# Kernel tuning notes

Hardware: AMD Instinct MI355X
Metric: run time of the kernel (lower is better)

The kernel has to match this reference:

```python
import jax, jax.numpy as jnp
import numpy as np

N = 50000       # nodes
E = 500000      # edges
F_IN = 64       # input feature dim
F_OUT = 64      # hidden/output dim
K = 3           # diffusion filter order
C = F_IN + F_OUT  # concat dim seen by each DConv


def _xavier(k, shape):
    fan_in, fan_out = shape[-2], shape[-1]
    lim = float(np.sqrt(6.0 / (fan_in + fan_out)))
    return jax.random.uniform(k, shape, jnp.float32, -lim, lim)


def setup_inputs() -> dict:
    key = jax.random.key(0)
    ks = jax.random.split(key, 8)
    X = jax.random.normal(ks[0], (N, F_IN), jnp.float32)
    H = jax.random.normal(ks[1], (N, F_OUT), jnp.float32)
    # ring edges guarantee every node has in-degree >= 1 and out-degree >= 1
    base = jnp.arange(N, dtype=jnp.int32)
    row = jnp.concatenate([base, jax.random.randint(ks[2], (E - N,), 0, N, jnp.int32)])
    col = jnp.concatenate([jnp.roll(base, 1), jax.random.randint(ks[3], (E - N,), 0, N, jnp.int32)])
    edge_index = jnp.stack([row, col])  # [2, E]
    W_z = _xavier(ks[4], (2, K, C, F_OUT))
    W_r = _xavier(ks[5], (2, K, C, F_OUT))
    W_h = _xavier(ks[6], (2, K, C, F_OUT))
    b = jnp.zeros((F_OUT,), jnp.float32)
    return {"X": X, "edge_index": edge_index, "H": H,
            "W_z": W_z, "b_z": b, "W_r": W_r, "b_r": b, "W_h": W_h, "b_h": b}


def _dconv(Xc, row, col, norm_out, norm_in, W, b):
    # PyG propagate: gather source (row) features, scale by edge norm, scatter-add to target (col)
    def prop(x, norm):
        return jax.ops.segment_sum(norm[:, None] * x[row], col, num_segments=N)
    Tx_0 = Xc
    Hout = Xc @ (W[0, 0] + W[1, 0])
    Tx_1_o = prop(Xc, norm_out)
    Tx_1_i = prop(Xc, norm_in)
    Hout = Hout + Tx_1_o @ W[0, 1] + Tx_1_i @ W[1, 1]
    for k in range(2, K):
        Tx_2_o = 2.0 * prop(Tx_1_o, norm_out) - Tx_0
        Tx_2_i = 2.0 * prop(Tx_1_i, norm_in) - Tx_0
        Hout = Hout + Tx_2_o @ W[0, k] + Tx_2_i @ W[1, k]
        # faithful to original: Tx_1 is never reassigned, so Tx_0 stays Xc
        Tx_0, Tx_1_o, Tx_1_i = Xc, Tx_2_o, Tx_2_i
    return Hout + b


def reference(X, edge_index, H, W_z, b_z, W_r, b_r, W_h, b_h):
    row, col = edge_index[0], edge_index[1]
    deg_out = jnp.zeros((N,), jnp.float32).at[row].add(1.0)
    deg_in = jnp.zeros((N,), jnp.float32).at[col].add(1.0)
    norm_out = (1.0 / deg_out)[row]
    norm_in = (1.0 / deg_in)[row]
    XH = jnp.concatenate([X, H], axis=1)
    Z = jax.nn.sigmoid(_dconv(XH, row, col, norm_out, norm_in, W_z, b_z))
    R = jax.nn.sigmoid(_dconv(XH, row, col, norm_out, norm_in, W_r, b_r))
    XHR = jnp.concatenate([X, H * R], axis=1)
    H_tilde = jnp.tanh(_dconv(XHR, row, col, norm_out, norm_in, W_h, b_h))
    H_new = Z * H + (1.0 - Z) * H_tilde
    # NaN infill with mean of non-NaN entries (faithful to original)
    mask = jnp.isnan(H_new)
    H_new = jnp.where(mask, jnp.nanmean(H_new), H_new)
    return H_new
```

## Files before the change

kernel.cpp:

```cpp
#include <hip/hip_runtime.h>
#include <hip/hip_bf16.h>
#include <math.h>

#define N_NODES 50000
#define N_EDGES 500000
#define C_DIM 128
#define N_TILES 3125

#define CSR_BLOCKS 1954
#define CONCAT_BLOCKS 3125
#define PACK_BLOCKS 480

typedef __attribute__((ext_vector_type(8))) short bf8;
typedef __attribute__((ext_vector_type(4))) float f32x4;
typedef __attribute__((ext_vector_type(2))) float f32x2;

__device__ __forceinline__ float bflo(unsigned u) { return __uint_as_float(u << 16); }
__device__ __forceinline__ float bfhi(unsigned u) { return __uint_as_float(u & 0xffff0000u); }
__device__ __forceinline__ unsigned short f2bfu(float f) {
    __hip_bfloat16 h = __float2bfloat16(f);
    unsigned short u;
    __builtin_memcpy(&u, &h, 2);
    return u;
}
__device__ __forceinline__ unsigned packbf(float a, float b) {
    return ((unsigned)f2bfu(b) << 16) | f2bfu(a);
}


__global__ void count_deg(const int* __restrict__ row, const int* __restrict__ col,
                          int* __restrict__ dout, int* __restrict__ din, int e) {
    int i = blockIdx.x * blockDim.x + threadIdx.x;
    if (i >= e) return;
    atomicAdd(&dout[row[i]], 1);
    atomicAdd(&din[col[i]], 1);
}

__global__ void scan_block(const int* __restrict__ counts, int* __restrict__ excl,
                           int* __restrict__ blocksums, int n) {
    __shared__ int tmp[1024];
    int tid = threadIdx.x;
    int gid = blockIdx.x * 1024 + tid;
    int v = (gid < n) ? counts[gid] : 0;
    tmp[tid] = v;
    __syncthreads();
    for (int off = 1; off < 1024; off <<= 1) {
        int t = (tid >= off) ? tmp[tid - off] : 0;
        __syncthreads();
        tmp[tid] += t;
        __syncthreads();
    }
    int incl = tmp[tid];
    if (gid < n) excl[gid] = incl - v;
    if (tid == 1023) blocksums[blockIdx.x] = incl;
}

__global__ void scan_sums(int* __restrict__ blocksums, int nb) {
    __shared__ int tmp[64];
    int tid = threadIdx.x;
    int v = (tid < nb) ? blocksums[tid] : 0;
    tmp[tid] = v;
    __syncthreads();
    for (int off = 1; off < 64; off <<= 1) {
        int t = (tid >= off) ? tmp[tid - off] : 0;
        __syncthreads();
        tmp[tid] += t;
        __syncthreads();
    }
    if (tid < nb) blocksums[tid] = tmp[tid] - v;
}

__global__ void scan_add(int* __restrict__ rowptr, const int* __restrict__ blocksums,
                         int* __restrict__ cursor, const int* __restrict__ dout,
                         const int* __restrict__ din, float2* __restrict__ winv,
                         int n, int e_total) {
    int gid = blockIdx.x * blockDim.x + threadIdx.x;
    if (gid < n) {
        int v = rowptr[gid] + blocksums[gid >> 10];
        rowptr[gid] = v;
        cursor[gid] = v;
        winv[gid] = make_float2(1.0f / (float)dout[gid], 1.0f / (float)din[gid]);
    }
    if (gid == n) rowptr[n] = e_total;
}

__device__ __forceinline__ float wraw(const float* W, int d, int kk, int k, int j) {
    return W[((d * 3 + kk) * 128 + k) * 64 + j];
}

__device__ __forceinline__ float zr_val(const float* Wz, const float* Wr, int k, int nn) {
    const float* W = (nn < 64) ? Wz : Wr;
    int j = nn & 63;
    if (k < 128) return wraw(W, 0, 0, k, j) + wraw(W, 1, 0, k, j);
    int k2 = k - 128;
    int kk = (k2 >= 256) ? 2 : 1;
    int k3 = k2 & 255;
    int p = k3 >> 2, sub = k3 & 3;
    return wraw(W, sub >> 1, kk, 2 * p + (sub & 1), j);
}

__device__ __forceinline__ float h_val(const float* Wh, int k, int j) {
    if (k < 64) return wraw(Wh, 0, 0, k, j) + wraw(Wh, 1, 0, k, j);
    if (k < 320) {
        int k2 = k - 64;
        int kk = (k2 >= 128) ? 2 : 1;
        int k3 = k2 & 127;
        int p = k3 >> 2, sub = k3 & 3;
        return wraw(Wh, sub >> 1, kk, 2 * p + (sub & 1), j);
    }
    if (k < 384) return wraw(Wh, 0, 0, 64 + (k - 320), j) + wraw(Wh, 1, 0, 64 + (k - 320), j);
    int k2 = k - 384;
    int kk = (k2 >= 128) ? 2 : 1;
    int k3 = k2 & 127;
    int p = k3 >> 2, sub = k3 & 3;
    return wraw(Wh, sub >> 1, kk, 64 + 2 * p + (sub & 1), j);
}

__global__ void fused_prep(const int* __restrict__ row, const int* __restrict__ col,
                           const float2* __restrict__ winv, int* __restrict__ cursor,
                           int* __restrict__ csr_src, float2* __restrict__ csr_w,
                           const float* __restrict__ X, const float* __restrict__ Hm,
                           unsigned short* __restrict__ XH, unsigned short* __restrict__ XHp,
                           const float* Wz, const float* Wr,
                           const float* Wh,
                           unsigned short* __restrict__ Wzrf, unsigned short* __restrict__ Whf,
                           int n, int e) {
    int b = blockIdx.x;
    if (b < CSR_BLOCKS) {
        int i = b * 256 + threadIdx.x;
        if (i >= e) return;
        int r = row[i], c = col[i];
        int pos = atomicAdd(&cursor[c], 1);
        csr_src[pos] = r;
        csr_w[pos] = winv[r];
    } else if (b < CSR_BLOCKS + CONCAT_BLOCKS) {
        int t = (b - CSR_BLOCKS) * 256 + threadIdx.x;
        int node = t >> 4, p = t & 15;
        const float* src = (p < 8) ? (X + (size_t)node * 64 + 8 * p)
                                   : (Hm + (size_t)node * 64 + 8 * (p - 8));
        float4 v0 = *(const float4*)src;
        float4 v1 = *(const float4*)(src + 4);
        uint4 o;
        o.x = packbf(v0.x, v0.y); o.y = packbf(v0.z, v0.w);
        o.z = packbf(v1.x, v1.y); o.w = packbf(v1.z, v1.w);
        *(uint4*)(XH + (size_t)node * 128 + 8 * p) = o;
        int tile = node >> 4, lr = node & 15, ck = p >> 2, q = p & 3;
        *(uint4*)(XHp + (((size_t)tile * 4 + ck) * 64 + q * 16 + lr) * 8) = o;
    } else {
        int i = (b - CSR_BLOCKS - CONCAT_BLOCKS) * 256 + threadIdx.x;
        if (i < 20 * 8 * 64 * 8) {
            int j = i & 7, lane = (i >> 3) & 63, nt = (i >> 9) & 7, ks = i >> 12;
            int k = ks * 32 + (lane >> 4) * 8 + j;
            int nn = nt * 16 + (lane & 15);
            Wzrf[i] = f2bfu(zr_val(Wz, Wr, k, nn));
        } else if (i < 20 * 8 * 64 * 8 + 20 * 4 * 64 * 8) {
            int i2 = i - 20 * 8 * 64 * 8;
            int j = i2 & 7, lane = (i2 >> 3) & 63, nt = (i2 >> 9) & 3, ks = i2 >> 11;
            int k = ks * 32 + (lane >> 4) * 8 + j;
            int nn = nt * 16 + (lane & 15);
            Whf[i2] = f2bfu(h_val(Wh, k, nn));
        }
    }
}


__global__ void prop1_128(const unsigned short* __restrict__ S,
                          const int* __restrict__ rowptr, const int* __restrict__ src,
                          const float2* __restrict__ w,
                          unsigned char* __restrict__ P18, unsigned short* __restrict__ P1p,
                          int n) {
    int tid = blockIdx.x * blockDim.x + threadIdx.x;
    int lane = tid & 63;
    int node = ((tid >> 6) << 1) + (lane >> 5);
    int p = lane & 31;
    if (node >= n) return;
    int beg = rowptr[node], end = rowptr[node + 1];
    float ao0 = 0.f, ao1 = 0.f, ao2 = 0.f, ao3 = 0.f;
    float ai0 = 0.f, ai1 = 0.f, ai2 = 0.f, ai3 = 0.f;
    int j = beg;
#define P1STEP(s_, w_) {                                                     \
        uint2 u = *(const uint2*)(S + (size_t)(s_) * 128 + 4 * p);           \
        float c0 = bflo(u.x), c1 = bfhi(u.x), c2 = bflo(u.y), c3 = bfhi(u.y);\
        ao0 = fmaf(w_.x, c0, ao0); ao1 = fmaf(w_.x, c1, ao1);                \
        ao2 = fmaf(w_.x, c2, ao2); ao3 = fmaf(w_.x, c3, ao3);                \
        ai0 = fmaf(w_.y, c0, ai0); ai1 = fmaf(w_.y, c1, ai1);                \
        ai2 = fmaf(w_.y, c2, ai2); ai3 = fmaf(w_.y, c3, ai3); }
    for (; j + 8 <= end; j += 8) {
        int s0 = src[j], s1 = src[j + 1], s2 = src[j + 2], s3 = src[j + 3];
        int s4 = src[j + 4], s5 = src[j + 5], s6 = src[j + 6], s7 = src[j + 7];
        float2 w0 = w[j], w1 = w[j + 1], w2 = w[j + 2], w3 = w[j + 3];
        float2 w4 = w[j + 4], w5 = w[j + 5], w6 = w[j + 6], w7 = w[j + 7];
        P1STEP(s0, w0); P1STEP(s1, w1); P1STEP(s2, w2); P1STEP(s3, w3);
        P1STEP(s4, w4); P1STEP(s5, w5); P1STEP(s6, w6); P1STEP(s7, w7);
    }
    for (; j + 4 <= end; j += 4) {
        int s0 = src[j], s1 = src[j + 1], s2 = src[j + 2], s3 = src[j + 3];
        float2 w0 = w[j], w1 = w[j + 1], w2 = w[j + 2], w3 = w[j + 3];
        P1STEP(s0, w0); P1STEP(s1, w1); P1STEP(s2, w2); P1STEP(s3, w3);
    }
    for (; j < end; ++j) {
        int s = src[j]; float2 wv = w[j];
        P1STEP(s, wv);
    }
#undef P1STEP
    unsigned wa = (unsigned)__builtin_amdgcn_cvt_pk_fp8_f32(ao0, ao1, 0, false);
    wa = (unsigned)__builtin_amdgcn_cvt_pk_fp8_f32(ai0, ai1, wa, true);
    unsigned wb = (unsigned)__builtin_amdgcn_cvt_pk_fp8_f32(ao2, ao3, 0, false);
    wb = (unsigned)__builtin_amdgcn_cvt_pk_fp8_f32(ai2, ai3, wb, true);
    uint2 o8; o8.x = wa; o8.y = wb;
    *(uint2*)(P18 + (size_t)node * 256 + 8 * p) = o8;
    uint4 o;
    o.x = packbf(ao0, ao1); o.y = packbf(ai0, ai1);
    o.z = packbf(ao2, ao3); o.w = packbf(ai2, ai3);
    int tile = node >> 4, lr = node & 15, ck = p >> 2, q = p & 3;
    *(uint4*)(P1p + (((size_t)tile * 8 + ck) * 64 + q * 16 + lr) * 8) = o;
}

__global__ void prop2_128(const unsigned char* __restrict__ P18,
                          const unsigned short* __restrict__ Xc,
                          const int* __restrict__ rowptr, const int* __restrict__ src,
                          const float2* __restrict__ w,
                          unsigned short* __restrict__ P2p, int n) {
    int tid = blockIdx.x * blockDim.x + threadIdx.x;
    int lane = tid & 63;
    int node = ((tid >> 6) << 1) + (lane >> 5);
    int p = lane & 31;
    if (node >= n) return;
    int beg = rowptr[node], end = rowptr[node + 1];
    float oa = 0.f, ob = 0.f, oc = 0.f, od = 0.f;
    float ia = 0.f, ib = 0.f, ic = 0.f, id = 0.f;
    int j = beg;
#define P2STEP(s_, w_) {                                                     \
        uint2 v = *(const uint2*)(P18 + (size_t)(s_) * 256 + 8 * p);         \
        f32x2 f0 = __builtin_amdgcn_cvt_pk_f32_fp8(v.x, false);              \
        f32x2 f1 = __builtin_amdgcn_cvt_pk_f32_fp8(v.x, true);               \
        f32x2 f2 = __builtin_amdgcn_cvt_pk_f32_fp8(v.y, false);              \
        f32x2 f3 = __builtin_amdgcn_cvt_pk_f32_fp8(v.y, true);               \
        oa = fmaf(w_.x, f0[0], oa); ob = fmaf(w_.x, f0[1], ob);              \
        ia = fmaf(w_.y, f1[0], ia); ib = fmaf(w_.y, f1[1], ib);              \
        oc = fmaf(w_.x, f2[0], oc); od = fmaf(w_.x, f2[1], od);              \
        ic = fmaf(w_.y, f3[0], ic); id = fmaf(w_.y, f3[1], id); }
    for (; j + 8 <= end; j += 8) {
        int s0 = src[j], s1 = src[j + 1], s2 = src[j + 2], s3 = src[j + 3];
        int s4 = src[j + 4], s5 = src[j + 5], s6 = src[j + 6], s7 = src[j + 7];
        float2 w0 = w[j], w1 = w[j + 1], w2 = w[j + 2], w3 = w[j + 3];
        float2 w4 = w[j + 4], w5 = w[j + 5], w6 = w[j + 6], w7 = w[j + 7];
        P2STEP(s0, w0); P2STEP(s1, w1); P2STEP(s2, w2); P2STEP(s3, w3);
        P2STEP(s4, w4); P2STEP(s5, w5); P2STEP(s6, w6); P2STEP(s7, w7);
    }
    for (; j + 4 <= end; j += 4) {
        int s0 = src[j], s1 = src[j + 1], s2 = src[j + 2], s3 = src[j + 3];
        float2 w0 = w[j], w1 = w[j + 1], w2 = w[j + 2], w3 = w[j + 3];
        P2STEP(s0, w0); P2STEP(s1, w1); P2STEP(s2, w2); P2STEP(s3, w3);
    }
    for (; j < end; ++j) {
        int s = src[j]; float2 wv = w[j];
        P2STEP(s, wv);
    }
#undef P2STEP
    uint2 ux = *(const uint2*)(Xc + (size_t)node * 128 + 4 * p);
    float xa = bflo(ux.x), xb = bfhi(ux.x), xc = bflo(ux.y), xd = bfhi(ux.y);
    uint4 o;
    o.x = packbf(2.f * oa - xa, 2.f * ob - xb);
    o.y = packbf(2.f * ia - xa, 2.f * ib - xb);
    o.z = packbf(2.f * oc - xc, 2.f * od - xd);
    o.w = packbf(2.f * ic - xc, 2.f * id - xd);
    int tile = node >> 4, lr = node & 15, ck = p >> 2, q = p & 3;
    *(uint4*)(P2p + (((size_t)tile * 8 + ck) * 64 + q * 16 + lr) * 8) = o;
}

__global__ void prop1_64(const unsigned short* __restrict__ HR,
                         const int* __restrict__ rowptr, const int* __restrict__ src,
                         const float2* __restrict__ w,
                         unsigned char* __restrict__ Q18, unsigned short* __restrict__ Q1p,
                         int n) {
    int tid = blockIdx.x * blockDim.x + threadIdx.x;
    int lane = tid & 63;
    int node = ((tid >> 6) << 2) + (lane >> 4);
    int p = lane & 15;
    if (node >= n) return;
    int beg = rowptr[node], end = rowptr[node + 1];
    float ao0 = 0.f, ao1 = 0.f, ao2 = 0.f, ao3 = 0.f;
    float ai0 = 0.f, ai1 = 0.f, ai2 = 0.f, ai3 = 0.f;
    int j = beg;
#define Q1STEP(s_, w_) {                                                     \
        uint2 u = *(const uint2*)(HR + (size_t)(s_) * 64 + 4 * p);           \
        float c0 = bflo(u.x), c1 = bfhi(u.x), c2 = bflo(u.y), c3 = bfhi(u.y);\
        ao0 = fmaf(w_.x, c0, ao0); ao1 = fmaf(w_.x, c1, ao1);                \
        ao2 = fmaf(w_.x, c2, ao2); ao3 = fmaf(w_.x, c3, ao3);                \
        ai0 = fmaf(w_.y, c0, ai0); ai1 = fmaf(w_.y, c1, ai1);                \
        ai2 = fmaf(w_.y, c2, ai2); ai3 = fmaf(w_.y, c3, ai3); }
    for (; j + 8 <= end; j += 8) {
        int s0 = src[j], s1 = src[j + 1], s2 = src[j + 2], s3 = src[j + 3];
        int s4 = src[j + 4], s5 = src[j + 5], s6 = src[j + 6], s7 = src[j + 7];
        float2 w0 = w[j], w1 = w[j + 1], w2 = w[j + 2], w3 = w[j + 3];
        float2 w4 = w[j + 4], w5 = w[j + 5], w6 = w[j + 6], w7 = w[j + 7];
        Q1STEP(s0, w0); Q1STEP(s1, w1); Q1STEP(s2, w2); Q1STEP(s3, w3);
        Q1STEP(s4, w4); Q1STEP(s5, w5); Q1STEP(s6, w6); Q1STEP(s7, w7);
    }
    for (; j + 4 <= end; j += 4) {
        int s0 = src[j], s1 = src[j + 1], s2 = src[j + 2], s3 = src[j + 3];
        float2 w0 = w[j], w1 = w[j + 1], w2 = w[j + 2], w3 = w[j + 3];
        Q1STEP(s0, w0); Q1STEP(s1, w1); Q1STEP(s2, w2); Q1STEP(s3, w3);
    }
    for (; j < end; ++j) {
        int s = src[j]; float2 wv = w[j];
        Q1STEP(s, wv);
    }
#undef Q1STEP
    unsigned wa = (unsigned)__builtin_amdgcn_cvt_pk_fp8_f32(ao0, ao1, 0, false);
    wa = (unsigned)__builtin_amdgcn_cvt_pk_fp8_f32(ai0, ai1, wa, true);
    unsigned wb = (unsigned)__builtin_amdgcn_cvt_pk_fp8_f32(ao2, ao3, 0, false);
    wb = (unsigned)__builtin_amdgcn_cvt_pk_fp8_f32(ai2, ai3, wb, true);
    uint2 o8; o8.x = wa; o8.y = wb;
    *(uint2*)(Q18 + (size_t)node * 128 + 8 * p) = o8;
    uint4 o;
    o.x = packbf(ao0, ao1); o.y = packbf(ai0, ai1);
    o.z = packbf(ao2, ao3); o.w = packbf(ai2, ai3);
    int tile = node >> 4, lr = node & 15, ck = p >> 2, q = p & 3;
    *(uint4*)(Q1p + (((size_t)tile * 4 + ck) * 64 + q * 16 + lr) * 8) = o;
}

__global__ void prop2_64(const unsigned char* __restrict__ Q18,
                         const unsigned short* __restrict__ HR,
                         const int* __restrict__ rowptr, const int* __restrict__ src,
                         const float2* __restrict__ w,
                         unsigned short* __restrict__ Q2p, int n) {
    int tid = blockIdx.x * blockDim.x + threadIdx.x;
    int lane = tid & 63;
    int node = ((tid >> 6) << 2) + (lane >> 4);
    int p = lane & 15;
    if (node >= n) return;
    int beg = rowptr[node], end = rowptr[node + 1];
    float oa = 0.f, ob = 0.f, oc = 0.f, od = 0.f;
    float ia = 0.f, ib = 0.f, ic = 0.f, id = 0.f;
    int j = beg;
#define Q2STEP(s_, w_) {                                                     \
        uint2 v = *(const uint2*)(Q18 + (size_t)(s_) * 128 + 8 * p);         \
        f32x2 f0 = __builtin_amdgcn_cvt_pk_f32_fp8(v.x, false);              \
        f32x2 f1 = __builtin_amdgcn_cvt_pk_f32_fp8(v.x, true);               \
        f32x2 f2 = __builtin_amdgcn_cvt_pk_f32_fp8(v.y, false);              \
        f32x2 f3 = __builtin_amdgcn_cvt_pk_f32_fp8(v.y, true);               \
        oa = fmaf(w_.x, f0[0], oa); ob = fmaf(w_.x, f0[1], ob);              \
        ia = fmaf(w_.y, f1[0], ia); ib = fmaf(w_.y, f1[1], ib);              \
        oc = fmaf(w_.x, f2[0], oc); od = fmaf(w_.x, f2[1], od);              \
        ic = fmaf(w_.y, f3[0], ic); id = fmaf(w_.y, f3[1], id); }
    for (; j + 8 <= end; j += 8) {
        int s0 = src[j], s1 = src[j + 1], s2 = src[j + 2], s3 = src[j + 3];
        int s4 = src[j + 4], s5 = src[j + 5], s6 = src[j + 6], s7 = src[j + 7];
        float2 w0 = w[j], w1 = w[j + 1], w2 = w[j + 2], w3 = w[j + 3];
        float2 w4 = w[j + 4], w5 = w[j + 5], w6 = w[j + 6], w7 = w[j + 7];
        Q2STEP(s0, w0); Q2STEP(s1, w1); Q2STEP(s2, w2); Q2STEP(s3, w3);
        Q2STEP(s4, w4); Q2STEP(s5, w5); Q2STEP(s6, w6); Q2STEP(s7, w7);
    }
    for (; j + 4 <= end; j += 4) {
        int s0 = src[j], s1 = src[j + 1], s2 = src[j + 2], s3 = src[j + 3];
        float2 w0 = w[j], w1 = w[j + 1], w2 = w[j + 2], w3 = w[j + 3];
        Q2STEP(s0, w0); Q2STEP(s1, w1); Q2STEP(s2, w2); Q2STEP(s3, w3);
    }
    for (; j < end; ++j) {
        int s = src[j]; float2 wv = w[j];
        Q2STEP(s, wv);
    }
#undef Q2STEP
    uint2 ux = *(const uint2*)(HR + (size_t)node * 64 + 4 * p);
    float xa = bflo(ux.x), xb = bfhi(ux.x), xc = bflo(ux.y), xd = bfhi(ux.y);
    uint4 o;
    o.x = packbf(2.f * oa - xa, 2.f * ob - xb);
    o.y = packbf(2.f * ia - xa, 2.f * ib - xb);
    o.z = packbf(2.f * oc - xc, 2.f * od - xd);
    o.w = packbf(2.f * ic - xc, 2.f * id - xd);
    int tile = node >> 4, lr = node & 15, ck = p >> 2, q = p & 3;
    *(uint4*)(Q2p + (((size_t)tile * 4 + ck) * 64 + q * 16 + lr) * 8) = o;
}


__global__ __launch_bounds__(256) void gemm_zr_mfma(
    const unsigned short* __restrict__ XHp, const unsigned short* __restrict__ P1p,
    const unsigned short* __restrict__ P2p,
    const unsigned short* __restrict__ Wf, const float* bz,
    const float* br, const float* __restrict__ H,
    float* __restrict__ Zf, unsigned short* __restrict__ HR, int n) {
    int tid = threadIdx.x;
    int lane = tid & 63;
    int ngrp = tid >> 6;
    int rowbase = blockIdx.x * 64;
    int lr = lane & 15, quad = lane >> 4;

    int tiles[4];
#pragma unroll
    for (int mt = 0; mt < 4; ++mt) {
        int t = (rowbase >> 4) + mt;
        tiles[mt] = (t > N_TILES - 1) ? N_TILES - 1 : t;
    }

    f32x4 zero = {0.f, 0.f, 0.f, 0.f};
    f32x4 acc[4][2];
#pragma unroll
    for (int a = 0; a < 4; ++a)
#pragma unroll
        for (int b = 0; b < 2; ++b) acc[a][b] = zero;

#pragma unroll
    for (int ks = 0; ks < 20; ++ks) {
        const unsigned short* T = (ks < 4) ? XHp : (ks < 12) ? P1p : P2p;
        int ck = (ks < 4) ? ks : (ks < 12) ? ks - 4 : ks - 12;
        int nck = (ks < 4) ? 4 : 8;
        bf8 b0 = *(const bf8*)(Wf + (((size_t)ks * 8 + ngrp * 2 + 0) * 64 + lane) * 8);
        bf8 b1 = *(const bf8*)(Wf + (((size_t)ks * 8 + ngrp * 2 + 1) * 64 + lane) * 8);
#pragma unroll
        for (int mt = 0; mt < 4; ++mt) {
            bf8 a = *(const bf8*)(T + (((size_t)tiles[mt] * nck + ck) * 64 + lane) * 8);
            acc[mt][0] = __builtin_amdgcn_mfma_f32_16x16x32_bf16(a, b0, acc[mt][0], 0, 0, 0);
            acc[mt][1] = __builtin_amdgcn_mfma_f32_16x16x32_bf16(a, b1, acc[mt][1], 0, 0, 0);
        }
    }
#pragma unroll
    for (int mt = 0; mt < 4; ++mt)
#pragma unroll
        for (int reg = 0; reg < 4; ++reg) {
            int r = rowbase + mt * 16 + quad * 4 + reg;
            if (r >= n) continue;
#pragma unroll
            for (int nt = 0; nt < 2; ++nt) {
                int cidx = ngrp * 32 + nt * 16 + lr;
                float bias = (cidx < 64) ? bz[cidx] : br[cidx - 64];
                float v = acc[mt][nt][reg] + bias;
                float s = 1.f / (1.f + expf(-v));
                if (cidx < 64) {
                    Zf[(size_t)r * 64 + cidx] = s;
                } else {
                    int c2 = cidx - 64;
                    HR[(size_t)r * 64 + c2] = f2bfu(H[(size_t)r * 64 + c2] * s);
                }
            }
        }
}

__global__ __launch_bounds__(256) void gemm_h_mfma(
    const unsigned short* __restrict__ XHp, const unsigned short* __restrict__ P1p,
    const unsigned short* __restrict__ P2p, const unsigned short* __restrict__ HR,
    const unsigned short* __restrict__ Q1p, const unsigned short* __restrict__ Q2p,
    const unsigned short* __restrict__ Wf, const float* bh,
    const float* __restrict__ Zf, const float* __restrict__ H,
    float* __restrict__ out, int n) {
    int tid = threadIdx.x;
    int lane = tid & 63;
    int wid = tid >> 6;
    int mh = wid & 1, ngrp = wid >> 1;
    int rowbase = blockIdx.x * 128 + mh * 64;
    int lr = lane & 15, quad = lane >> 4;

    int tiles[4];
    const unsigned short* hrp[4];
#pragma unroll
    for (int mt = 0; mt < 4; ++mt) {
        int t = (rowbase >> 4) + mt;
        tiles[mt] = (t > N_TILES - 1) ? N_TILES - 1 : t;
        int r = rowbase + mt * 16 + lr;
        if (r >= n) r = n - 1;
        hrp[mt] = HR + (size_t)r * 64 + quad * 8;
    }

    f32x4 zero = {0.f, 0.f, 0.f, 0.f};
    f32x4 acc[4][2];
#pragma unroll
    for (int a = 0; a < 4; ++a)
#pragma unroll
        for (int b = 0; b < 2; ++b) acc[a][b] = zero;

#pragma unroll
    for (int ks = 0; ks < 20; ++ks) {
        bf8 b0 = *(const bf8*)(Wf + (((size_t)ks * 4 + ngrp * 2 + 0) * 64 + lane) * 8);
        bf8 b1 = *(const bf8*)(Wf + (((size_t)ks * 4 + ngrp * 2 + 1) * 64 + lane) * 8);
#pragma unroll
        for (int mt = 0; mt < 4; ++mt) {
            bf8 a;
            if (ks == 10 || ks == 11) {
                a = *(const bf8*)(hrp[mt] + (ks - 10) * 32);
            } else {
                const unsigned short* T = (ks < 2) ? XHp : (ks < 6) ? P1p :
                                          (ks < 10) ? P2p : (ks < 16) ? Q1p : Q2p;
                int ck = (ks < 2) ? ks : (ks < 6) ? ks - 2 : (ks < 10) ? ks - 6 :
                         (ks < 16) ? ks - 12 : ks - 16;
                int nck = (ks < 2) ? 4 : (ks < 10) ? 8 : 4;
                a = *(const bf8*)(T + (((size_t)tiles[mt] * nck + ck) * 64 + lane) * 8);
            }
            acc[mt][0] = __builtin_amdgcn_mfma_f32_16x16x32_bf16(a, b0, acc[mt][0], 0, 0, 0);
            acc[mt][1] = __builtin_amdgcn_mfma_f32_16x16x32_bf16(a, b1, acc[mt][1], 0, 0, 0);
        }
    }
#pragma unroll
    for (int mt = 0; mt < 4; ++mt)
#pragma unroll
        for (int reg = 0; reg < 4; ++reg) {
            int r = rowbase + mt * 16 + quad * 4 + reg;
            if (r >= n) continue;
#pragma unroll
            for (int nt = 0; nt < 2; ++nt) {
                int cidx = ngrp * 32 + nt * 16 + lr;
                float ht = tanhf(acc[mt][nt][reg] + bh[cidx]);
                float z = Zf[(size_t)r * 64 + cidx];
                float h_old = H[(size_t)r * 64 + cidx];
                out[(size_t)r * 64 + cidx] = z * h_old + (1.f - z) * ht;
            }
        }
}


static inline size_t rup(size_t x) { return (x + 63) & ~(size_t)63; }

extern "C" void kernel_launch(void* const* d_in, const int* in_sizes, int n_in,
                              void* d_out, int out_size, void* d_ws, size_t ws_size,
                              hipStream_t stream) {
    const float* X  = (const float*)d_in[0];
    const int*   EI = (const int*)d_in[1];
    const float* H  = (const float*)d_in[2];
    const float* Wz = (const float*)d_in[3];
    const float* bz = (const float*)d_in[4];
    const float* Wr = (const float*)d_in[5];
    const float* br = (const float*)d_in[6];
    const float* Wh = (const float*)d_in[7];
    const float* bh = (const float*)d_in[8];
    float* out = (float*)d_out;

    const int* row = EI;
    const int* col = EI + N_EDGES;

    char* ws = (char*)d_ws;
    size_t off = 0;
    auto carve = [&](size_t bytes) { void* p = ws + off; off += rup(bytes); return p; };

    int*   deg_out   = (int*)carve(N_NODES * 4);
    int*   deg_in    = (int*)carve(N_NODES * 4);
    int*   rowptr    = (int*)carve((N_NODES + 1) * 4);
    int*   cursor    = (int*)carve(N_NODES * 4);
    int*   blocksums = (int*)carve(64 * 4);
    float2* winv     = (float2*)carve(N_NODES * 8);
    int*   csr_src   = (int*)carve(N_EDGES * 4);
    float2* csr_w    = (float2*)carve(N_EDGES * 8);
    unsigned short* XH  = (unsigned short*)carve((size_t)N_NODES * 128 * 2);
    unsigned char*  Pscr = (unsigned char*)carve((size_t)N_NODES * 256 + (size_t)N_TILES * 4 * 512 * 2);
    unsigned short* XHp = (unsigned short*)carve((size_t)N_TILES * 4 * 512 * 2);
    unsigned short* P1p = (unsigned short*)carve((size_t)N_TILES * 8 * 512 * 2);
    unsigned short* P2p = (unsigned short*)carve((size_t)N_TILES * 8 * 512 * 2);
    unsigned short* HR  = (unsigned short*)carve((size_t)N_NODES * 64 * 2);
    float* Zf           = (float*)carve((size_t)N_NODES * 64 * 4);
    unsigned short* Wzrf = (unsigned short*)carve(20 * 8 * 64 * 8 * 2);
    unsigned short* Whf  = (unsigned short*)carve(20 * 4 * 64 * 8 * 2);

    unsigned char*  P18 = Pscr;
    unsigned char*  Q18 = (unsigned char*)XH;
    unsigned short* Q1p = (unsigned short*)Pscr;
    unsigned short* Q2p = (unsigned short*)(Pscr + (size_t)N_NODES * 256);

    hipMemsetAsync(deg_out, 0, rup(N_NODES * 4) + rup(N_NODES * 4), stream);
    count_deg<<<(N_EDGES + 255) / 256, 256, 0, stream>>>(row, col, deg_out, deg_in, N_EDGES);

    int nblk = (N_NODES + 1023) / 1024;
    scan_block<<<nblk, 1024, 0, stream>>>(deg_in, rowptr, blocksums, N_NODES);
    scan_sums<<<1, 64, 0, stream>>>(blocksums, nblk);
    scan_add<<<(N_NODES + 1 + 255) / 256, 256, 0, stream>>>(rowptr, blocksums, cursor,
                                                            deg_out, deg_in, winv, N_NODES, N_EDGES);

    fused_prep<<<CSR_BLOCKS + CONCAT_BLOCKS + PACK_BLOCKS, 256, 0, stream>>>(
        row, col, winv, cursor, csr_src, csr_w,
        X, H, XH, XHp, Wz, Wr, Wh, Wzrf, Whf, N_NODES, N_EDGES);

    int blocks_p128 = (((N_NODES + 1) / 2) * 64 + 255) / 256;
    prop1_128<<<blocks_p128, 256, 0, stream>>>(XH, rowptr, csr_src, csr_w, P18, P1p, N_NODES);
    prop2_128<<<blocks_p128, 256, 0, stream>>>(P18, XH, rowptr, csr_src, csr_w, P2p, N_NODES);

    int zr_blocks = (N_NODES + 63) / 64;
    gemm_zr_mfma<<<zr_blocks, 256, 0, stream>>>(XHp, P1p, P2p, Wzrf, bz, br, H, Zf, HR, N_NODES);

    int blocks_p64 = (((N_NODES + 3) / 4) * 64 + 255) / 256;
    prop1_64<<<blocks_p64, 256, 0, stream>>>(HR, rowptr, csr_src, csr_w, Q18, Q1p, N_NODES);
    prop2_64<<<blocks_p64, 256, 0, stream>>>(Q18, HR, rowptr, csr_src, csr_w, Q2p, N_NODES);

    int h_blocks = (N_NODES + 127) / 128;
    gemm_h_mfma<<<h_blocks, 256, 0, stream>>>(XHp, P1p, P2p, HR, Q1p, Q2p,
                                              Whf, bh, Zf, H, out, N_NODES);
}
```

Measured before the change: 343.0 us.

## Drop per-edge CSR weights, shrink GEMM row tiles, and prefetch MFMA operands

The per-edge csr_w array is removed. Each propagation kernel now reads the per-node winv[src] directly, which saves the scatter write in fused_prep and an 8-byte stream per edge, at the cost of an extra dependent gather per edge. Both MFMA GEMM kernels now cover fewer rows per block (32 instead of 64/128), so more blocks launch and fewer accumulators are held per wave. They also prefetch the next k-step's A/B fragments into registers before issuing the current MFMAs, to hide load latency.

```diff
diff --git a/kernel.cpp b/kernel.cpp
--- a/kernel.cpp
+++ b/kernel.cpp
@@ -117,8 +117,8 @@
 }
 
 __global__ void fused_prep(const int* __restrict__ row, const int* __restrict__ col,
-                           const float2* __restrict__ winv, int* __restrict__ cursor,
-                           int* __restrict__ csr_src, float2* __restrict__ csr_w,
+                           int* __restrict__ cursor,
+                           int* __restrict__ csr_src,
                            const float* __restrict__ X, const float* __restrict__ Hm,
                            unsigned short* __restrict__ XH, unsigned short* __restrict__ XHp,
                            const float* Wz, const float* Wr,
@@ -132,7 +132,6 @@
         int r = row[i], c = col[i];
         int pos = atomicAdd(&cursor[c], 1);
         csr_src[pos] = r;
-        csr_w[pos] = winv[r];
     } else if (b < CSR_BLOCKS + CONCAT_BLOCKS) {
         int t = (b - CSR_BLOCKS) * 256 + threadIdx.x;
         int node = t >> 4, p = t & 15;
@@ -166,7 +165,7 @@
 
 __global__ void prop1_128(const unsigned short* __restrict__ S,
                           const int* __restrict__ rowptr, const int* __restrict__ src,
-                          const float2* __restrict__ w,
+                          const float2* __restrict__ winv,
                           unsigned char* __restrict__ P18, unsigned short* __restrict__ P1p,
                           int n) {
     int tid = blockIdx.x * blockDim.x + threadIdx.x;
@@ -188,18 +187,18 @@
     for (; j + 8 <= end; j += 8) {
         int s0 = src[j], s1 = src[j + 1], s2 = src[j + 2], s3 = src[j + 3];
         int s4 = src[j + 4], s5 = src[j + 5], s6 = src[j + 6], s7 = src[j + 7];
-        float2 w0 = w[j], w1 = w[j + 1], w2 = w[j + 2], w3 = w[j + 3];
-        float2 w4 = w[j + 4], w5 = w[j + 5], w6 = w[j + 6], w7 = w[j + 7];
+        float2 w0 = winv[s0], w1 = winv[s1], w2 = winv[s2], w3 = winv[s3];
+        float2 w4 = winv[s4], w5 = winv[s5], w6 = winv[s6], w7 = winv[s7];
         P1STEP(s0, w0); P1STEP(s1, w1); P1STEP(s2, w2); P1STEP(s3, w3);
         P1STEP(s4, w4); P1STEP(s5, w5); P1STEP(s6, w6); P1STEP(s7, w7);
     }
     for (; j + 4 <= end; j += 4) {
         int s0 = src[j], s1 = src[j + 1], s2 = src[j + 2], s3 = src[j + 3];
-        float2 w0 = w[j], w1 = w[j + 1], w2 = w[j + 2], w3 = w[j + 3];
+        float2 w0 = winv[s0], w1 = winv[s1], w2 = winv[s2], w3 = winv[s3];
         P1STEP(s0, w0); P1STEP(s1, w1); P1STEP(s2, w2); P1STEP(s3, w3);
     }
     for (; j < end; ++j) {
-        int s = src[j]; float2 wv = w[j];
+        int s = src[j]; float2 wv = winv[s];
         P1STEP(s, wv);
     }
 #undef P1STEP
@@ -219,7 +218,7 @@
 __global__ void prop2_128(const unsigned char* __restrict__ P18,
                           const unsigned short* __restrict__ Xc,
                           const int* __restrict__ rowptr, const int* __restrict__ src,
-                          const float2* __restrict__ w,
+                          const float2* __restrict__ winv,
                           unsigned short* __restrict__ P2p, int n) {
     int tid = blockIdx.x * blockDim.x + threadIdx.x;
     int lane = tid & 63;
@@ -243,18 +242,18 @@
     for (; j + 8 <= end; j += 8) {
         int s0 = src[j], s1 = src[j + 1], s2 = src[j + 2], s3 = src[j + 3];
         int s4 = src[j + 4], s5 = src[j + 5], s6 = src[j + 6], s7 = src[j + 7];
-        float2 w0 = w[j], w1 = w[j + 1], w2 = w[j + 2], w3 = w[j + 3];
-        float2 w4 = w[j + 4], w5 = w[j + 5], w6 = w[j + 6], w7 = w[j + 7];
+        float2 w0 = winv[s0], w1 = winv[s1], w2 = winv[s2], w3 = winv[s3];
+        float2 w4 = winv[s4], w5 = winv[s5], w6 = winv[s6], w7 = winv[s7];
         P2STEP(s0, w0); P2STEP(s1, w1); P2STEP(s2, w2); P2STEP(s3, w3);
         P2STEP(s4, w4); P2STEP(s5, w5); P2STEP(s6, w6); P2STEP(s7, w7);
     }
     for (; j + 4 <= end; j += 4) {
         int s0 = src[j], s1 = src[j + 1], s2 = src[j + 2], s3 = src[j + 3];
-        float2 w0 = w[j], w1 = w[j + 1], w2 = w[j + 2], w3 = w[j + 3];
+        float2 w0 = winv[s0], w1 = winv[s1], w2 = winv[s2], w3 = winv[s3];
         P2STEP(s0, w0); P2STEP(s1, w1); P2STEP(s2, w2); P2STEP(s3, w3);
     }
     for (; j < end; ++j) {
-        int s = src[j]; float2 wv = w[j];
+        int s = src[j]; float2 wv = winv[s];
         P2STEP(s, wv);
     }
 #undef P2STEP
@@ -271,7 +270,7 @@
 
 __global__ void prop1_64(const unsigned short* __restrict__ HR,
                          const int* __restrict__ rowptr, const int* __restrict__ src,
-                         const float2* __restrict__ w,
+                         const float2* __restrict__ winv,
                          unsigned char* __restrict__ Q18, unsigned short* __restrict__ Q1p,
                          int n) {
     int tid = blockIdx.x * blockDim.x + threadIdx.x;
@@ -293,18 +292,18 @@
     for (; j + 8 <= end; j += 8) {
         int s0 = src[j], s1 = src[j + 1], s2 = src[j + 2], s3 = src[j + 3];
         int s4 = src[j + 4], s5 = src[j + 5], s6 = src[j + 6], s7 = src[j + 7];
-        float2 w0 = w[j], w1 = w[j + 1], w2 = w[j + 2], w3 = w[j + 3];
-        float2 w4 = w[j + 4], w5 = w[j + 5], w6 = w[j + 6], w7 = w[j + 7];
+        float2 w0 = winv[s0], w1 = winv[s1], w2 = winv[s2], w3 = winv[s3];
+        float2 w4 = winv[s4], w5 = winv[s5], w6 = winv[s6], w7 = winv[s7];
         Q1STEP(s0, w0); Q1STEP(s1, w1); Q1STEP(s2, w2); Q1STEP(s3, w3);
         Q1STEP(s4, w4); Q1STEP(s5, w5); Q1STEP(s6, w6); Q1STEP(s7, w7);
     }
     for (; j + 4 <= end; j += 4) {
         int s0 = src[j], s1 = src[j + 1], s2 = src[j + 2], s3 = src[j + 3];
-        float2 w0 = w[j], w1 = w[j + 1], w2 = w[j + 2], w3 = w[j + 3];
+        float2 w0 = winv[s0], w1 = winv[s1], w2 = winv[s2], w3 = winv[s3];
         Q1STEP(s0, w0); Q1STEP(s1, w1); Q1STEP(s2, w2); Q1STEP(s3, w3);
     }
     for (; j < end; ++j) {
-        int s = src[j]; float2 wv = w[j];
+        int s = src[j]; float2 wv = winv[s];
         Q1STEP(s, wv);
     }
 #undef Q1STEP
@@ -324,7 +323,7 @@
 __global__ void prop2_64(const unsigned char* __restrict__ Q18,
                          const unsigned short* __restrict__ HR,
                          const int* __restrict__ rowptr, const int* __restrict__ src,
-                         const float2* __restrict__ w,
+                         const float2* __restrict__ winv,
                          unsigned short* __restrict__ Q2p, int n) {
     int tid = blockIdx.x * blockDim.x + threadIdx.x;
     int lane = tid & 63;
@@ -348,18 +347,18 @@
     for (; j + 8 <= end; j += 8) {
         int s0 = src[j], s1 = src[j + 1], s2 = src[j + 2], s3 = src[j + 3];
         int s4 = src[j + 4], s5 = src[j + 5], s6 = src[j + 6], s7 = src[j + 7];
-        float2 w0 = w[j], w1 = w[j + 1], w2 = w[j + 2], w3 = w[j + 3];
-        float2 w4 = w[j + 4], w5 = w[j + 5], w6 = w[j + 6], w7 = w[j + 7];
+        float2 w0 = winv[s0], w1 = winv[s1], w2 = winv[s2], w3 = winv[s3];
+        float2 w4 = winv[s4], w5 = winv[s5], w6 = winv[s6], w7 = winv[s7];
         Q2STEP(s0, w0); Q2STEP(s1, w1); Q2STEP(s2, w2); Q2STEP(s3, w3);
         Q2STEP(s4, w4); Q2STEP(s5, w5); Q2STEP(s6, w6); Q2STEP(s7, w7);
     }
     for (; j + 4 <= end; j += 4) {
         int s0 = src[j], s1 = src[j + 1], s2 = src[j + 2], s3 = src[j + 3];
-        float2 w0 = w[j], w1 = w[j + 1], w2 = w[j + 2], w3 = w[j + 3];
+        float2 w0 = winv[s0], w1 = winv[s1], w2 = winv[s2], w3 = winv[s3];
         Q2STEP(s0, w0); Q2STEP(s1, w1); Q2STEP(s2, w2); Q2STEP(s3, w3);
     }
     for (; j < end; ++j) {
-        int s = src[j]; float2 wv = w[j];
+        int s = src[j]; float2 wv = winv[s];
         Q2STEP(s, wv);
     }
 #undef Q2STEP
@@ -384,39 +383,49 @@
     int tid = threadIdx.x;
     int lane = tid & 63;
     int ngrp = tid >> 6;
-    int rowbase = blockIdx.x * 64;
+    int rowbase = blockIdx.x * 32;
     int lr = lane & 15, quad = lane >> 4;
 
-    int tiles[4];
-#pragma unroll
-    for (int mt = 0; mt < 4; ++mt) {
+    int tiles[2];
+#pragma unroll
+    for (int mt = 0; mt < 2; ++mt) {
         int t = (rowbase >> 4) + mt;
         tiles[mt] = (t > N_TILES - 1) ? N_TILES - 1 : t;
     }
 
-    f32x4 zero = {0.f, 0.f, 0.f, 0.f};
-    f32x4 acc[4][2];
-#pragma unroll
-    for (int a = 0; a < 4; ++a)
-#pragma unroll
-        for (int b = 0; b < 2; ++b) acc[a][b] = zero;
-
-#pragma unroll
-    for (int ks = 0; ks < 20; ++ks) {
+    auto LDB = [&](int ks, int nt) {
+        return *(const bf8*)(Wf + (((size_t)ks * 8 + ngrp * 2 + nt) * 64 + lane) * 8);
+    };
+    auto LDA = [&](int ks, int mt) {
         const unsigned short* T = (ks < 4) ? XHp : (ks < 12) ? P1p : P2p;
         int ck = (ks < 4) ? ks : (ks < 12) ? ks - 4 : ks - 12;
         int nck = (ks < 4) ? 4 : 8;
-        bf8 b0 = *(const bf8*)(Wf + (((size_t)ks * 8 + ngrp * 2 + 0) * 64 + lane) * 8);
-        bf8 b1 = *(const bf8*)(Wf + (((size_t)ks * 8 + ngrp * 2 + 1) * 64 + lane) * 8);
-#pragma unroll
-        for (int mt = 0; mt < 4; ++mt) {
-            bf8 a = *(const bf8*)(T + (((size_t)tiles[mt] * nck + ck) * 64 + lane) * 8);
-            acc[mt][0] = __builtin_amdgcn_mfma_f32_16x16x32_bf16(a, b0, acc[mt][0], 0, 0, 0);
-            acc[mt][1] = __builtin_amdgcn_mfma_f32_16x16x32_bf16(a, b1, acc[mt][1], 0, 0, 0);
+        return *(const bf8*)(T + (((size_t)tiles[mt] * nck + ck) * 64 + lane) * 8);
+    };
+
+    f32x4 zero = {0.f, 0.f, 0.f, 0.f};
+    f32x4 acc[2][2];
+#pragma unroll
+    for (int a = 0; a < 2; ++a)
+#pragma unroll
+        for (int b = 0; b < 2; ++b) acc[a][b] = zero;
+
+    bf8 a0 = LDA(0, 0), a1 = LDA(0, 1), b0 = LDB(0, 0), b1 = LDB(0, 1);
+#pragma unroll
+    for (int ks = 0; ks < 20; ++ks) {
+        bf8 na0, na1, nb0, nb1;
+        if (ks < 19) {
+            na0 = LDA(ks + 1, 0); na1 = LDA(ks + 1, 1);
+            nb0 = LDB(ks + 1, 0); nb1 = LDB(ks + 1, 1);
         }
-    }
-#pragma unroll
-    for (int mt = 0; mt < 4; ++mt)
+        acc[0][0] = __builtin_amdgcn_mfma_f32_16x16x32_bf16(a0, b0, acc[0][0], 0, 0, 0);
+        acc[0][1] = __builtin_amdgcn_mfma_f32_16x16x32_bf16(a0, b1, acc[0][1], 0, 0, 0);
+        acc[1][0] = __builtin_amdgcn_mfma_f32_16x16x32_bf16(a1, b0, acc[1][0], 0, 0, 0);
+        acc[1][1] = __builtin_amdgcn_mfma_f32_16x16x32_bf16(a1, b1, acc[1][1], 0, 0, 0);
+        if (ks < 19) { a0 = na0; a1 = na1; b0 = nb0; b1 = nb1; }
+    }
+#pragma unroll
+    for (int mt = 0; mt < 2; ++mt)
 #pragma unroll
         for (int reg = 0; reg < 4; ++reg) {
             int r = rowbase + mt * 16 + quad * 4 + reg;
@@ -448,63 +457,58 @@
     int lane = tid & 63;
     int wid = tid >> 6;
     int mh = wid & 1, ngrp = wid >> 1;
-    int rowbase = blockIdx.x * 128 + mh * 64;
+    int rowbase = blockIdx.x * 32 + mh * 16;
     int lr = lane & 15, quad = lane >> 4;
 
-    int tiles[4];
-    const unsigned short* hrp[4];
-#pragma unroll
-    for (int mt = 0; mt < 4; ++mt) {
-        int t = (rowbase >> 4) + mt;
-        tiles[mt] = (t > N_TILES - 1) ? N_TILES - 1 : t;
-        int r = rowbase + mt * 16 + lr;
-        if (r >= n) r = n - 1;
-        hrp[mt] = HR + (size_t)r * 64 + quad * 8;
-    }
+    int t = rowbase >> 4;
+    int tile = (t > N_TILES - 1) ? N_TILES - 1 : t;
+    int rh = rowbase + lr;
+    if (rh >= n) rh = n - 1;
+    const unsigned short* hrp = HR + (size_t)rh * 64 + quad * 8;
+
+    auto LDB = [&](int ks, int nt) {
+        return *(const bf8*)(Wf + (((size_t)ks * 4 + ngrp * 2 + nt) * 64 + lane) * 8);
+    };
+    auto LDA = [&](int ks) {
+        if (ks == 10 || ks == 11) {
+            return *(const bf8*)(hrp + (ks - 10) * 32);
+        }
+        const unsigned short* T = (ks < 2) ? XHp : (ks < 6) ? P1p :
+                                  (ks < 10) ? P2p : (ks < 16) ? Q1p : Q2p;
+        int ck = (ks < 2) ? ks : (ks < 6) ? ks - 2 : (ks < 10) ? ks - 6 :
+                 (ks < 16) ? ks - 12 : ks - 16;
+        int nck = (ks < 2) ? 4 : (ks < 10) ? 8 : 4;
+        return *(const bf8*)(T + (((size_t)tile * nck + ck) * 64 + lane) * 8);
+    };
 
     f32x4 zero = {0.f, 0.f, 0.f, 0.f};
-    f32x4 acc[4][2];
-#pragma unroll
-    for (int a = 0; a < 4; ++a)
-#pragma unroll
-        for (int b = 0; b < 2; ++b) acc[a][b] = zero;
-
+    f32x4 acc[2];
+    acc[0] = zero; acc[1] = zero;
+
+    bf8 a0 = LDA(0), b0 = LDB(0, 0), b1 = LDB(0, 1);
 #pragma unroll
     for (int ks = 0; ks < 20; ++ks) {
-        bf8 b0 = *(const bf8*)(Wf + (((size_t)ks * 4 + ngrp * 2 + 0) * 64 + lane) * 8);
-        bf8 b1 = *(const bf8*)(Wf + (((size_t)ks * 4 + ngrp * 2 + 1) * 64 + lane) * 8);
-#pragma unroll
-        for (int mt = 0; mt < 4; ++mt) {
-            bf8 a;
-            if (ks == 10 || ks == 11) {
-                a = *(const bf8*)(hrp[mt] + (ks - 10) * 32);
-            } else {
-                const unsigned short* T = (ks < 2) ? XHp : (ks < 6) ? P1p :
-                                          (ks < 10) ? P2p : (ks < 16) ? Q1p : Q2p;
-                int ck = (ks < 2) ? ks : (ks < 6) ? ks - 2 : (ks < 10) ? ks - 6 :
-                         (ks < 16) ? ks - 12 : ks - 16;
-                int nck = (ks < 2) ? 4 : (ks < 10) ? 8 : 4;
-                a = *(const bf8*)(T + (((size_t)tiles[mt] * nck + ck) * 64 + lane) * 8);
-            }
-            acc[mt][0] = __builtin_amdgcn_mfma_f32_16x16x32_bf16(a, b0, acc[mt][0], 0, 0, 0);
-            acc[mt][1] = __builtin_amdgcn_mfma_f32_16x16x32_bf16(a, b1, acc[mt][1], 0, 0, 0);
+        bf8 na0, nb0, nb1;
+        if (ks < 19) {
+            na0 = LDA(ks + 1); nb0 = LDB(ks + 1, 0); nb1 = LDB(ks + 1, 1);
         }
-    }
-#pragma unroll
-    for (int mt = 0; mt < 4; ++mt)
-#pragma unroll
-        for (int reg = 0; reg < 4; ++reg) {
-            int r = rowbase + mt * 16 + quad * 4 + reg;
-            if (r >= n) continue;
-#pragma unroll
-            for (int nt = 0; nt < 2; ++nt) {
-                int cidx = ngrp * 32 + nt * 16 + lr;
-                float ht = tanhf(acc[mt][nt][reg] + bh[cidx]);
-                float z = Zf[(size_t)r * 64 + cidx];
-                float h_old = H[(size_t)r * 64 + cidx];
-                out[(size_t)r * 64 + cidx] = z * h_old + (1.f - z) * ht;
-            }
+        acc[0] = __builtin_amdgcn_mfma_f32_16x16x32_bf16(a0, b0, acc[0], 0, 0, 0);
+        acc[1] = __builtin_amdgcn_mfma_f32_16x16x32_bf16(a0, b1, acc[1], 0, 0, 0);
+        if (ks < 19) { a0 = na0; b0 = nb0; b1 = nb1; }
+    }
+#pragma unroll
+    for (int reg = 0; reg < 4; ++reg) {
+        int r = rowbase + quad * 4 + reg;
+        if (r >= n) continue;
+#pragma unroll
+        for (int nt = 0; nt < 2; ++nt) {
+            int cidx = ngrp * 32 + nt * 16 + lr;
+            float ht = tanhf(acc[nt][reg] + bh[cidx]);
+            float z = Zf[(size_t)r * 64 + cidx];
+            float h_old = H[(size_t)r * 64 + cidx];
+            out[(size_t)r * 64 + cidx] = z * h_old + (1.f - z) * ht;
         }
+    }
 }
 
 
@@ -538,7 +542,6 @@
     int*   blocksums = (int*)carve(64 * 4);
     float2* winv     = (float2*)carve(N_NODES * 8);
     int*   csr_src   = (int*)carve(N_EDGES * 4);
-    float2* csr_w    = (float2*)carve(N_EDGES * 8);
     unsigned short* XH  = (unsigned short*)carve((size_t)N_NODES * 128 * 2);
     unsigned char*  Pscr = (unsigned char*)carve((size_t)N_NODES * 256 + (size_t)N_TILES * 4 * 512 * 2);
     unsigned short* XHp = (unsigned short*)carve((size_t)N_TILES * 4 * 512 * 2);
@@ -564,21 +567,21 @@
                                                             deg_out, deg_in, winv, N_NODES, N_EDGES);
 
     fused_prep<<<CSR_BLOCKS + CONCAT_BLOCKS + PACK_BLOCKS, 256, 0, stream>>>(
-        row, col, winv, cursor, csr_src, csr_w,
+        row, col, cursor, csr_src,
         X, H, XH, XHp, Wz, Wr, Wh, Wzrf, Whf, N_NODES, N_EDGES);
 
     int blocks_p128 = (((N_NODES + 1) / 2) * 64 + 255) / 256;
-    prop1_128<<<blocks_p128, 256, 0, stream>>>(XH, rowptr, csr_src, csr_w, P18, P1p, N_NODES);
-    prop2_128<<<blocks_p128, 256, 0, stream>>>(P18, XH, rowptr, csr_src, csr_w, P2p, N_NODES);
-
-    int zr_blocks = (N_NODES + 63) / 64;
+    prop1_128<<<blocks_p128, 256, 0, stream>>>(XH, rowptr, csr_src, winv, P18, P1p, N_NODES);
+    prop2_128<<<blocks_p128, 256, 0, stream>>>(P18, XH, rowptr, csr_src, winv, P2p, N_NODES);
+
+    int zr_blocks = (N_NODES + 31) / 32;
     gemm_zr_mfma<<<zr_blocks, 256, 0, stream>>>(XHp, P1p, P2p, Wzrf, bz, br, H, Zf, HR, N_NODES);
 
     int blocks_p64 = (((N_NODES + 3) / 4) * 64 + 255) / 256;
-    prop1_64<<<blocks_p64, 256, 0, stream>>>(HR, rowptr, csr_src, csr_w, Q18, Q1p, N_NODES);
-    prop2_64<<<blocks_p64, 256, 0, stream>>>(Q18, HR, rowptr, csr_src, csr_w, Q2p, N_NODES);
-
-    int h_blocks = (N_NODES + 127) / 128;
+    prop1_64<<<blocks_p64, 256, 0, stream>>>(HR, rowptr, csr_src, winv, Q18, Q1p, N_NODES);
+    prop2_64<<<blocks_p64, 256, 0, stream>>>(Q18, HR, rowptr, csr_src, winv, Q2p, N_NODES);
+
+    int h_blocks = (N_NODES + 31) / 32;
     gemm_h_mfma<<<h_blocks, 256, 0, stream>>>(XHp, P1p, P2p, HR, Q1p, Q2p,
                                               Whf, bh, Zf, H, out, N_NODES);
 }
```

Measured after the change: 328.9 us. 1.04x faster.
